# Kernel optimization log

Measured on AMD Instinct MI355X. Metric: run time of the kernel, lower is better.

The kernel has to match this reference:

```python
import jax, jax.numpy as jnp
import numpy as np

B, S, D, H = 8, 512, 2048, 16
DOWN, UP, R = 512, 2048, 512
HD = D // H        # 128, used only in the additive scale
VHD = UP // H      # 128, content head dim / value head dim
BASE = 10000.0


def _rope_tables(head_dim):
    # Faithful to source: positions span arange(head_dim), NOT max_len.
    pos = jnp.arange(head_dim, dtype=jnp.float32)
    div = jnp.exp(jnp.arange(0, head_dim, 2, dtype=jnp.float32) * (-np.log(BASE) / head_dim))
    theta = jnp.outer(pos, div)          # [head_dim, head_dim//2]
    return jnp.sin(theta), jnp.cos(theta)


def _apply_rope(q, num_heads, head_dim):
    # q: [B, S, num_heads*head_dim] -> [B, num_heads, S, head_dim] with interleaved rotation
    b, s, _ = q.shape
    q = q.reshape(b, s, num_heads, head_dim).transpose(0, 2, 1, 3)
    sin, cos = _rope_tables(head_dim)
    sin = sin[:s][None, None]            # [1,1,S,head_dim//2]
    cos = cos[:s][None, None]
    q_ = q.reshape(b, num_heads, s, head_dim // 2, 2)
    q1, q2 = q_[..., 0], q_[..., 1]
    o1 = q1 * cos - q2 * sin
    o2 = q2 * cos + q1 * sin
    return jnp.stack([o1, o2], axis=-1).reshape(b, num_heads, s, head_dim)


def setup_inputs() -> dict:
    key = jax.random.key(0)
    ks = jax.random.split(key, 18)
    w = lambda k, shp: jax.random.normal(k, shp, jnp.float32) * 0.02
    return {
        "X":    jax.random.normal(ks[0], (B, S, D), jnp.float32),
        "Wdq":  w(ks[1], (D, DOWN)),      "bdq":  w(ks[2], (DOWN,)),
        "Wdkv": w(ks[3], (D, DOWN)),      "bdkv": w(ks[4], (DOWN,)),
        "Wuq":  w(ks[5], (DOWN, UP)),     "buq":  w(ks[6], (UP,)),
        "Wuk":  w(ks[7], (DOWN, UP)),     "buk":  w(ks[8], (UP,)),
        "Wuv":  w(ks[9], (DOWN, UP)),     "buv":  w(ks[10], (UP,)),
        "Wqr":  w(ks[11], (DOWN, R * H)), "bqr":  w(ks[12], (R * H,)),
        "Wkr":  w(ks[13], (D, R)),        "bkr":  w(ks[14], (R,)),
        "Wfc":  w(ks[15], (VHD * H, D)),  "bfc":  w(ks[16], (D,)),
    }


def reference(X, Wdq, bdq, Wdkv, bdkv, Wuq, buq, Wuk, buk, Wuv, buv,
              Wqr, bqr, Wkr, bkr, Wfc, bfc):
    b, s, _ = X.shape
    c_q = X @ Wdq + bdq                                  # [B,S,DOWN]
    c_kv = X @ Wdkv + bdkv                               # [B,S,DOWN]
    q_c = (c_q @ Wuq + buq).reshape(b, s, H, VHD).transpose(0, 2, 1, 3)   # [B,H,S,VHD]
    k_c = (c_kv @ Wuk + buk).reshape(b, s, H, VHD).transpose(0, 2, 1, 3)
    v_c = (c_kv @ Wuv + buv).reshape(b, s, H, VHD).transpose(0, 2, 1, 3)
    q_r = _apply_rope(c_q @ Wqr + bqr, H, R)             # [B,H,S,R]
    k_r = _apply_rope(X @ Wkr + bkr, 1, R)               # [B,1,S,R]
    q = jnp.concatenate([q_c, q_r], axis=-1)             # [B,H,S,VHD+R]
    k = jnp.concatenate([k_c, jnp.broadcast_to(k_r, (b, H, s, R))], axis=-1)
    scale = HD ** 0.5 + R ** 0.5                         # additive scale, as in source
    scores = jnp.einsum('bhqd,bhkd->bhqk', q, k) / scale
    attn = jax.nn.softmax(scores, axis=-1)               # dropout: eval mode (identity)
    o = jnp.einsum('bhqk,bhkd->bhqd', attn, v_c).transpose(0, 2, 1, 3).reshape(b, s, H * VHD)
    return o @ Wfc + bfc
```

## Files before the change

### kernel.cpp

```cpp
#include <hip/hip_runtime.h>
#include <hip/hip_bf16.h>
#include <stdint.h>

typedef unsigned short u16;
typedef short bf16x8 __attribute__((ext_vector_type(8)));
typedef float f32x4 __attribute__((ext_vector_type(4)));

__device__ __forceinline__ float us2f(u16 u) {
    union { unsigned int i; float f; } x;
    x.i = ((unsigned int)u) << 16;
    return x.f;
}

__device__ __forceinline__ u16 f2us(float f) {
    union { float f; unsigned int i; } x; x.f = f;
    unsigned int lsb = (x.i >> 16) & 1u;
    x.i += 0x7FFFu + lsb;
    return (u16)(x.i >> 16);
}

__device__ __forceinline__ void gl_lds16(const u16* g, u16* l) {
    __builtin_amdgcn_global_load_lds(
        (const __attribute__((address_space(1))) void*)(uintptr_t)(const void*)g,
        (__attribute__((address_space(3))) void*)(uintptr_t)(void*)l,
        16, 0, 0);
}

#define FLAG_ROPE2  1
#define FLAG_TRANS2 4
#define FLAG_F32OUT 8

struct GArgs {
    const u16 *A0, *B0, *B0r2;
    int K0;
    const float* bias;
    void* C; void* C2;
    int colSplit;
};

template <int LDA0, int LDB0, int LDC, int LDC2, int FLAGS>
__global__ __launch_bounds__(256)
void gemm_mfma(GArgs g)
{
    __shared__ u16 As[128 * 64];
    __shared__ u16 Bs[128 * 64];

    const int t    = threadIdx.x;
    const int lane = t & 63;
    const int w    = t >> 6;
    const int wm   = w >> 1, wn = w & 1;
    const int m0   = blockIdx.y * 128;
    const int n0   = blockIdx.x * 128;
    const bool r2  = (n0 >= g.colSplit);

    const int srow = t >> 3;
    const int sp   = t & 7;
    u16* dA = As + t * 8;
    u16* dB = Bs + t * 8;

    const int lr = lane & 15;
    const int jj = lane >> 4;

    f32x4 acc[4][4];
#pragma unroll
    for (int i = 0; i < 4; ++i)
#pragma unroll
        for (int j = 0; j < 4; ++j)
            acc[i][j] = (f32x4){0.f, 0.f, 0.f, 0.f};

    {
        const u16* A = g.A0;
        const u16* B = r2 ? g.B0r2 - (long)g.colSplit * LDB0 : g.B0;
        const u16* gA[4];
        const u16* gB[4];
#pragma unroll
        for (int r = 0; r < 4; ++r) {
            int row = r * 32 + srow;
            int gc  = (sp - row) & 7;
            gA[r] = A + (long)(m0 + row) * LDA0 + gc * 8;
            gB[r] = B + (long)(n0 + row) * LDB0 + gc * 8;
        }
        for (int kt = 0; kt < g.K0; kt += 64) {
#pragma unroll
            for (int r = 0; r < 4; ++r) {
                gl_lds16(gA[r], dA + r * 2048);
                gl_lds16(gB[r], dB + r * 2048);
                gA[r] += 64; gB[r] += 64;
            }
            __syncthreads();
#pragma unroll
            for (int s = 0; s < 2; ++s) {
                bf16x8 af[4], bfr[4];
#pragma unroll
                for (int mi = 0; mi < 4; ++mi) {
                    int row  = wm * 64 + mi * 16 + lr;
                    int slot = (s * 4 + jj + row) & 7;
                    af[mi] = *(const bf16x8*)&As[row * 64 + slot * 8];
                }
#pragma unroll
                for (int ni = 0; ni < 4; ++ni) {
                    int row  = wn * 64 + ni * 16 + lr;
                    int slot = (s * 4 + jj + row) & 7;
                    bfr[ni] = *(const bf16x8*)&Bs[row * 64 + slot * 8];
                }
#pragma unroll
                for (int mi = 0; mi < 4; ++mi)
#pragma unroll
                    for (int ni = 0; ni < 4; ++ni)
                        acc[mi][ni] = __builtin_amdgcn_mfma_f32_16x16x32_bf16(
                            af[mi], bfr[ni], acc[mi][ni], 0, 0, 0);
            }
            __syncthreads();
        }
    }

    const int eCol0 = n0 + wn * 64 + lr;
    const int eRow0 = m0 + wm * 64 + jj * 4;
    const bool oddc = lane & 1;

    if (g.bias) {
#pragma unroll
        for (int ni = 0; ni < 4; ++ni) {
            float bv = g.bias[eCol0 + ni * 16];
#pragma unroll
            for (int mi = 0; mi < 4; ++mi) {
                acc[mi][ni][0] += bv; acc[mi][ni][1] += bv;
                acc[mi][ni][2] += bv; acc[mi][ni][3] += bv;
            }
        }
    }

    if (!r2) {
#pragma unroll
        for (int mi = 0; mi < 4; ++mi)
#pragma unroll
            for (int ni = 0; ni < 4; ++ni) {
                int rowb = eRow0 + mi * 16;
                int colg = eCol0 + ni * 16;
                if (FLAGS & FLAG_F32OUT) {
                    float* cp = (float*)g.C;
#pragma unroll
                    for (int i = 0; i < 4; ++i)
                        cp[(long)(rowb + i) * LDC + colg] = acc[mi][ni][i];
                } else {
                    u16* cp = (u16*)g.C;
#pragma unroll
                    for (int i = 0; i < 4; ++i)
                        cp[(long)(rowb + i) * LDC + colg] = f2us(acc[mi][ni][i]);
                }
            }
    } else if (FLAGS & FLAG_ROPE2) {
        const float base_s = (float)(eRow0 & 511);
#pragma unroll
        for (int ni = 0; ni < 4; ++ni) {
            int col2 = eCol0 + ni * 16 - g.colSplit;
            int rp   = (col2 & 511) & ~1;
            float f  = __expf(-9.2103403719761836f * (float)rp * (1.0f / 512.0f));
            float s1, c1, s16, c16, sb, cb;
            __sincosf(f, &s1, &c1);
            __sincosf(16.0f * f, &s16, &c16);
            __sincosf(base_s * f, &sb, &cb);
            float cm = cb, sm = sb;
#pragma unroll
            for (int mi = 0; mi < 4; ++mi) {
                f32x4 v = acc[mi][ni];
                float cr = cm, sr = sm;
#pragma unroll
                for (int i = 0; i < 4; ++i) {
                    float other = __shfl_xor(v[i], 1, 64);
                    v[i] = oddc ? (v[i] * cr + other * sr)
                                : (v[i] * cr - other * sr);
                    float cn = cr * c1 - sr * s1;
                    sr = sr * c1 + cr * s1; cr = cn;
                }
                int rowb = eRow0 + mi * 16;
                u16* cp = (u16*)g.C2;
#pragma unroll
                for (int i = 0; i < 4; ++i)
                    cp[(long)(rowb + i) * LDC2 + col2] = f2us(v[i]);
                float cn = cm * c16 - sm * s16;
                sm = sm * c16 + cm * s16; cm = cn;
            }
        }
    } else {
#pragma unroll
        for (int mi = 0; mi < 4; ++mi)
#pragma unroll
            for (int ni = 0; ni < 4; ++ni) {
                int rowb = eRow0 + mi * 16;
                int col2 = eCol0 + ni * 16 - g.colSplit;
                if (FLAGS & FLAG_TRANS2) {
                    u16* cp = (u16*)g.C2 + (long)col2 * LDC2 + rowb;
                    ushort4 o4;
                    o4.x = f2us(acc[mi][ni][0]); o4.y = f2us(acc[mi][ni][1]);
                    o4.z = f2us(acc[mi][ni][2]); o4.w = f2us(acc[mi][ni][3]);
                    *(ushort4*)cp = o4;
                } else {
                    u16* cp = (u16*)g.C2;
#pragma unroll
                    for (int i = 0; i < 4; ++i)
                        cp[(long)(rowb + i) * LDC2 + col2] = f2us(acc[mi][ni][i]);
                }
            }
    }
}

__global__ __launch_bounds__(256, 2)
void attn_fused(const u16* __restrict__ qc, const u16* __restrict__ kc,
                const u16* __restrict__ qr, const u16* __restrict__ kr,
                const u16* __restrict__ vt, u16* __restrict__ o)
{
    __shared__ u16 As[128 * 64];
    __shared__ u16 Bs[128 * 64];
    __shared__ u16 Ps[128 * 136];
    __shared__ float l_sum[128];

    const int t    = threadIdx.x;
    const int lane = t & 63;
    const int w    = t >> 6;
    const int wm   = w >> 1, wn = w & 1;
    const int m0   = blockIdx.x * 128;
    const int z    = blockIdx.y;
    const int bb   = z >> 4, h = z & 15;

    if (t < 128) l_sum[t] = 0.f;

    const int srow = t >> 3;
    const int sp   = t & 7;
    u16* dA = As + t * 8;
    u16* dB = Bs + t * 8;
    int rrow[4], rgc[4];
#pragma unroll
    for (int r = 0; r < 4; ++r) {
        rrow[r] = r * 32 + srow;
        rgc[r]  = (sp - rrow[r]) & 7;
    }

    const int lr = lane & 15;
    const int jj = lane >> 4;

    const u16* gqc[4];
    const u16* gqr[4];
#pragma unroll
    for (int r = 0; r < 4; ++r) {
        gqc[r] = qc + (long)(bb * 512 + m0 + rrow[r]) * 2048 + h * 128 + rgc[r] * 8;
        gqr[r] = qr + (long)(bb * 512 + m0 + rrow[r]) * 8192 + h * 512 + rgc[r] * 8;
    }

    f32x4 acc_o[4][4];
#pragma unroll
    for (int i = 0; i < 4; ++i)
#pragma unroll
        for (int j = 0; j < 4; ++j) acc_o[i][j] = (f32x4){0.f, 0.f, 0.f, 0.f};

    const float scale = 1.0f / 33.941125496954285f;

    for (int nt = 0; nt < 4; ++nt) {
        const int n0k = nt * 128;

        f32x4 acc_s[4][4];
#pragma unroll
        for (int i = 0; i < 4; ++i)
#pragma unroll
            for (int j = 0; j < 4; ++j) acc_s[i][j] = (f32x4){0.f, 0.f, 0.f, 0.f};

        const u16* pa[4];
        const u16* pb[4];
#pragma unroll
        for (int r = 0; r < 4; ++r) {
            pa[r] = gqc[r];
            pb[r] = kc + (long)(bb * 512 + n0k + rrow[r]) * 2048 + h * 128 + rgc[r] * 8;
        }
        for (int seg = 0; seg < 2; ++seg) {
            int iters = seg == 0 ? 2 : 8;
            for (int kt = 0; kt < iters; ++kt) {
#pragma unroll
                for (int r = 0; r < 4; ++r) {
                    gl_lds16(pa[r], dA + r * 2048);
                    gl_lds16(pb[r], dB + r * 2048);
                    pa[r] += 64; pb[r] += 64;
                }
                __syncthreads();
#pragma unroll
                for (int s = 0; s < 2; ++s) {
                    bf16x8 af[4], bfr[4];
#pragma unroll
                    for (int mi = 0; mi < 4; ++mi) {
                        int row  = wm * 64 + mi * 16 + lr;
                        int slot = (s * 4 + jj + row) & 7;
                        af[mi] = *(const bf16x8*)&As[row * 64 + slot * 8];
                    }
#pragma unroll
                    for (int ni = 0; ni < 4; ++ni) {
                        int row  = wn * 64 + ni * 16 + lr;
                        int slot = (s * 4 + jj + row) & 7;
                        bfr[ni] = *(const bf16x8*)&Bs[row * 64 + slot * 8];
                    }
#pragma unroll
                    for (int mi = 0; mi < 4; ++mi)
#pragma unroll
                        for (int ni = 0; ni < 4; ++ni)
                            acc_s[mi][ni] = __builtin_amdgcn_mfma_f32_16x16x32_bf16(
                                af[mi], bfr[ni], acc_s[mi][ni], 0, 0, 0);
                }
                __syncthreads();
            }
            if (seg == 0) {
#pragma unroll
                for (int r = 0; r < 4; ++r) {
                    pa[r] = gqr[r];
                    pb[r] = kr + (long)(bb * 512 + n0k + rrow[r]) * 1536 + rgc[r] * 8;
                }
            }
        }

#pragma unroll
        for (int mi = 0; mi < 4; ++mi) {
            float rowpart[4] = {0.f, 0.f, 0.f, 0.f};
#pragma unroll
            for (int ni = 0; ni < 4; ++ni) {
                f32x4 v = acc_s[mi][ni];
                int colP = wn * 64 + ni * 16 + lr;
#pragma unroll
                for (int i = 0; i < 4; ++i) {
                    float e = __expf(v[i] * scale);
                    rowpart[i] += e;
                    int rowP = wm * 64 + mi * 16 + jj * 4 + i;
                    Ps[rowP * 136 + colP] = f2us(e);
                }
            }
#pragma unroll
            for (int i = 0; i < 4; ++i) {
                float s4 = rowpart[i];
                s4 += __shfl_xor(s4, 1, 64);
                s4 += __shfl_xor(s4, 2, 64);
                s4 += __shfl_xor(s4, 4, 64);
                s4 += __shfl_xor(s4, 8, 64);
                if ((lane & 15) == 0)
                    atomicAdd(&l_sum[wm * 64 + mi * 16 + jj * 4 + i], s4);
            }
        }

        const u16* pv[4];
#pragma unroll
        for (int r = 0; r < 4; ++r)
            pv[r] = vt + (long)(h * 128 + rrow[r]) * 4096 + bb * 512 + n0k + rgc[r] * 8;
        for (int kt = 0; kt < 2; ++kt) {
#pragma unroll
            for (int r = 0; r < 4; ++r) {
                gl_lds16(pv[r], dB + r * 2048);
                pv[r] += 64;
            }
            __syncthreads();
#pragma unroll
            for (int s = 0; s < 2; ++s) {
                bf16x8 af[4], bfr[4];
#pragma unroll
                for (int mi = 0; mi < 4; ++mi) {
                    int row = wm * 64 + mi * 16 + lr;
                    af[mi] = *(const bf16x8*)&Ps[row * 136 + kt * 64 + s * 32 + jj * 8];
                }
#pragma unroll
                for (int ni = 0; ni < 4; ++ni) {
                    int row  = wn * 64 + ni * 16 + lr;
                    int slot = (s * 4 + jj + row) & 7;
                    bfr[ni] = *(const bf16x8*)&Bs[row * 64 + slot * 8];
                }
#pragma unroll
                for (int mi = 0; mi < 4; ++mi)
#pragma unroll
                    for (int ni = 0; ni < 4; ++ni)
                        acc_o[mi][ni] = __builtin_amdgcn_mfma_f32_16x16x32_bf16(
                            af[mi], bfr[ni], acc_o[mi][ni], 0, 0, 0);
            }
            __syncthreads();
        }
    }

#pragma unroll
    for (int mi = 0; mi < 4; ++mi) {
#pragma unroll
        for (int i = 0; i < 4; ++i) {
            int row = wm * 64 + mi * 16 + jj * 4 + i;
            float linv = 1.0f / l_sum[row];
            long grow = (long)(bb * 512 + m0 + row) * 2048 + h * 128;
#pragma unroll
            for (int ni = 0; ni < 4; ++ni) {
                int colc = wn * 64 + ni * 16 + lr;
                o[grow + colc] = f2us(acc_o[mi][ni][i] * linv);
            }
        }
    }
}

__global__ __launch_bounds__(256)
void conv_f32_bf16(const float* __restrict__ in, u16* __restrict__ out)
{
    int i = blockIdx.x * 256 + threadIdx.x;
    float4 v = ((const float4*)in)[i];
    ushort4 o;
    o.x = f2us(v.x); o.y = f2us(v.y); o.z = f2us(v.z); o.w = f2us(v.w);
    ((ushort4*)out)[i] = o;
}

struct TC3 { const float* in0; const float* in1; const float* in2;
             u16* out; long outStride; int K; int N; };

__global__ __launch_bounds__(256)
void tconv3(TC3 a)
{
    __shared__ float tile[32][33];
    const float* in = blockIdx.z == 0 ? a.in0 : (blockIdx.z == 1 ? a.in1 : a.in2);
    u16* out = a.out + blockIdx.z * a.outStride;
    int n0 = blockIdx.x * 32, k0 = blockIdx.y * 32;
    int c = threadIdx.x & 31, r0 = threadIdx.x >> 5;
#pragma unroll
    for (int j = 0; j < 4; ++j) {
        int r = r0 + j * 8;
        tile[r][c] = in[(long)(k0 + r) * a.N + n0 + c];
    }
    __syncthreads();
#pragma unroll
    for (int j = 0; j < 4; ++j) {
        int r = r0 + j * 8;
        out[(long)(n0 + r) * a.K + k0 + c] = f2us(tile[c][r]);
    }
}

extern "C" void kernel_launch(void* const* d_in, const int* in_sizes, int n_in,
                              void* d_out, int out_size, void* d_ws, size_t ws_size,
                              hipStream_t stream)
{
    (void)in_sizes; (void)n_in; (void)out_size; (void)ws_size;

    const float* X    = (const float*)d_in[0];
    const float* Wdq  = (const float*)d_in[1];  const float* bdq  = (const float*)d_in[2];
    const float* Wdkv = (const float*)d_in[3];  const float* bdkv = (const float*)d_in[4];
    const float* Wuq  = (const float*)d_in[5];  const float* buq  = (const float*)d_in[6];
    const float* Wuk  = (const float*)d_in[7];  const float* buk  = (const float*)d_in[8];
    const float* Wuv  = (const float*)d_in[9];  const float* buv  = (const float*)d_in[10];
    const float* Wqr  = (const float*)d_in[11]; const float* bqr  = (const float*)d_in[12];
    const float* Wkr  = (const float*)d_in[13]; const float* bkr  = (const float*)d_in[14];
    const float* Wfc  = (const float*)d_in[15]; const float* bfc  = (const float*)d_in[16];
    float* out = (float*)d_out;

    u16* ws = (u16*)d_ws;
    u16* Xb     = ws;
    u16* Wc1    = Xb   + 8388608;
    u16* Wc2    = Wc1  + 3145728;
    u16* Wqr_t  = Wc2  + 3145728;
    u16* Wfc_t  = Wqr_t + 4194304;
    u16* ckk    = Wfc_t + 4194304;
    u16* q_c    = ckk  + 6291456;
    u16* k_c    = q_c  + 8388608;
    u16* v_t    = k_c  + 8388608;
    u16* q_r    = v_t  + 8388608;
    u16* o      = q_r  + 33554432;
    float* biasD = (float*)(o + 8388608);
    float* biasQ = biasD + 1536;
    float* biasK = biasQ + 10240;

    dim3 blk(256, 1, 1);

    conv_f32_bf16<<<8192, blk, 0, stream>>>(X, Xb);
    {   TC3 a{Wdq, Wdkv, Wkr, Wc1, 1048576, 2048, 512};
        tconv3<<<dim3(16, 64, 3), blk, 0, stream>>>(a); }
    {   TC3 a{Wuq, Wuk, Wuv, Wc2, 1048576, 512, 2048};
        tconv3<<<dim3(64, 16, 3), blk, 0, stream>>>(a); }
    {   TC3 a{Wqr, nullptr, nullptr, Wqr_t, 0, 512, 8192};
        tconv3<<<dim3(256, 16, 1), blk, 0, stream>>>(a); }
    {   TC3 a{Wfc, nullptr, nullptr, Wfc_t, 0, 2048, 2048};
        tconv3<<<dim3(64, 64, 1), blk, 0, stream>>>(a); }
    hipMemcpyAsync(biasD,        bdq,  512 * 4,  hipMemcpyDeviceToDevice, stream);
    hipMemcpyAsync(biasD + 512,  bdkv, 512 * 4,  hipMemcpyDeviceToDevice, stream);
    hipMemcpyAsync(biasD + 1024, bkr,  512 * 4,  hipMemcpyDeviceToDevice, stream);
    hipMemcpyAsync(biasQ,        buq,  2048 * 4, hipMemcpyDeviceToDevice, stream);
    hipMemcpyAsync(biasQ + 2048, bqr,  8192 * 4, hipMemcpyDeviceToDevice, stream);
    hipMemcpyAsync(biasK,        buk,  2048 * 4, hipMemcpyDeviceToDevice, stream);
    hipMemcpyAsync(biasK + 2048, buv,  2048 * 4, hipMemcpyDeviceToDevice, stream);

    const int NOSPLIT = 1 << 30;

    {
        GArgs a{};
        a.A0 = Xb; a.B0 = Wc1; a.B0r2 = Wc1 + 2l * 1048576; a.K0 = 2048;
        a.bias = biasD; a.C = ckk; a.C2 = ckk + 1024;
        a.colSplit = 1024;
        gemm_mfma<2048, 2048, 1536, 1536, FLAG_ROPE2>
            <<<dim3(12, 32, 1), blk, 0, stream>>>(a);
    }
    {
        GArgs a{};
        a.A0 = ckk; a.B0 = Wc2; a.B0r2 = Wqr_t; a.K0 = 512;
        a.bias = biasQ; a.C = q_c; a.C2 = q_r;
        a.colSplit = 2048;
        gemm_mfma<1536, 512, 2048, 8192, FLAG_ROPE2>
            <<<dim3(80, 32, 1), blk, 0, stream>>>(a);
    }
    {
        GArgs a{};
        a.A0 = ckk + 512; a.B0 = Wc2 + 1048576; a.B0r2 = Wc2 + 2l * 1048576;
        a.K0 = 512;
        a.bias = biasK; a.C = k_c; a.C2 = v_t;
        a.colSplit = 2048;
        gemm_mfma<1536, 512, 2048, 4096, FLAG_TRANS2>
            <<<dim3(32, 32, 1), blk, 0, stream>>>(a);
    }

    attn_fused<<<dim3(4, 128, 1), blk, 0, stream>>>(
        q_c, k_c, q_r, ckk + 1024, v_t, o);

    {
        GArgs a{};
        a.A0 = o; a.B0 = Wfc_t; a.B0r2 = Wfc_t; a.K0 = 2048;
        a.bias = bfc; a.C = out; a.C2 = out;
        a.colSplit = NOSPLIT;
        gemm_mfma<2048, 2048, 2048, 1, FLAG_F32OUT>
            <<<dim3(16, 32, 1), blk, 0, stream>>>(a);
    }
}
```

Before: 466.7 us.

## Merge weight transposes and bias copies into single launches; XCD-aware attention block mapping

Four transpose-convert launches are merged into one flat-grid kernel, and seven device-to-device bias memcpys are replaced by a single gather kernel. Both cut launch and memcpy overhead. The attention kernel also remaps its block index so that all query tiles and heads of one batch land on the same XCD, which should improve L2 reuse of K/V. The remap assumes the attention grid is 4x128 and round-robin dispatch across eight XCDs.

```diff
diff --git a/kernel.cpp b/kernel.cpp
--- a/kernel.cpp
+++ b/kernel.cpp
@@ -219,8 +219,12 @@
     const int lane = t & 63;
     const int w    = t >> 6;
     const int wm   = w >> 1, wn = w & 1;
-    const int m0   = blockIdx.x * 128;
-    const int z    = blockIdx.y;
+
+    const int flat = blockIdx.x + (blockIdx.y << 2);
+    const int xcd  = flat & 7;
+    const int j    = flat >> 3;
+    const int m0   = (j >> 4) * 128;
+    const int z    = xcd * 16 + (j & 15);
     const int bb   = z >> 4, h = z & 15;
 
     if (t < 128) l_sum[t] = 0.f;
@@ -251,7 +255,7 @@
 #pragma unroll
     for (int i = 0; i < 4; ++i)
 #pragma unroll
-        for (int j = 0; j < 4; ++j) acc_o[i][j] = (f32x4){0.f, 0.f, 0.f, 0.f};
+        for (int j2 = 0; j2 < 4; ++j2) acc_o[i][j2] = (f32x4){0.f, 0.f, 0.f, 0.f};
 
     const float scale = 1.0f / 33.941125496954285f;
 
@@ -262,7 +266,7 @@
 #pragma unroll
         for (int i = 0; i < 4; ++i)
 #pragma unroll
-            for (int j = 0; j < 4; ++j) acc_s[i][j] = (f32x4){0.f, 0.f, 0.f, 0.f};
+            for (int j2 = 0; j2 < 4; ++j2) acc_s[i][j2] = (f32x4){0.f, 0.f, 0.f, 0.f};
 
         const u16* pa[4];
         const u16* pb[4];
@@ -403,27 +407,69 @@
     ((ushort4*)out)[i] = o;
 }
 
-struct TC3 { const float* in0; const float* in1; const float* in2;
-             u16* out; long outStride; int K; int N; };
+struct TCAll {
+    const float *Wdq, *Wdkv, *Wkr, *Wuq, *Wuk, *Wuv, *Wqr, *Wfc;
+    u16 *Wc1, *Wc2, *Wqr_t, *Wfc_t;
+};
 
 __global__ __launch_bounds__(256)
-void tconv3(TC3 a)
+void tconv_all(TCAll a)
 {
     __shared__ float tile[32][33];
-    const float* in = blockIdx.z == 0 ? a.in0 : (blockIdx.z == 1 ? a.in1 : a.in2);
-    u16* out = a.out + blockIdx.z * a.outStride;
-    int n0 = blockIdx.x * 32, k0 = blockIdx.y * 32;
-    int c = threadIdx.x & 31, r0 = threadIdx.x >> 5;
+    const int bid = blockIdx.x;
+    const float* in; u16* out; int K, N, nx, ny;
+    if (bid < 3072) {
+        int z = bid >> 10, rem = bid & 1023;
+        in = z == 0 ? a.Wdq : (z == 1 ? a.Wdkv : a.Wkr);
+        out = a.Wc1 + z * 1048576;
+        K = 2048; N = 512; nx = rem & 15; ny = rem >> 4;
+    } else if (bid < 6144) {
+        int l = bid - 3072, z = l >> 10, rem = l & 1023;
+        in = z == 0 ? a.Wuq : (z == 1 ? a.Wuk : a.Wuv);
+        out = a.Wc2 + z * 1048576;
+        K = 512; N = 2048; nx = rem & 63; ny = rem >> 6;
+    } else if (bid < 10240) {
+        int l = bid - 6144;
+        in = a.Wqr; out = a.Wqr_t;
+        K = 512; N = 8192; nx = l & 255; ny = l >> 8;
+    } else {
+        int l = bid - 10240;
+        in = a.Wfc; out = a.Wfc_t;
+        K = 2048; N = 2048; nx = l & 63; ny = l >> 6;
+    }
+    const int n0 = nx * 32, k0 = ny * 32;
+    const int c = threadIdx.x & 31, r0 = threadIdx.x >> 5;
 #pragma unroll
     for (int j = 0; j < 4; ++j) {
         int r = r0 + j * 8;
-        tile[r][c] = in[(long)(k0 + r) * a.N + n0 + c];
+        tile[r][c] = in[(long)(k0 + r) * N + n0 + c];
     }
     __syncthreads();
 #pragma unroll
     for (int j = 0; j < 4; ++j) {
         int r = r0 + j * 8;
-        out[(long)(n0 + r) * a.K + k0 + c] = f2us(tile[c][r]);
+        out[(long)(n0 + r) * K + k0 + c] = f2us(tile[c][r]);
+    }
+}
+
+struct BG {
+    const float *bdq, *bdkv, *bkr, *buq, *bqr, *buk, *buv;
+    float *biasD, *biasQ, *biasK;
+};
+
+__global__ __launch_bounds__(256)
+void bias_gather(BG a)
+{
+    int i = blockIdx.x * 256 + threadIdx.x;
+    if (i < 1536) {
+        float v = i < 512 ? a.bdq[i] : (i < 1024 ? a.bdkv[i - 512] : a.bkr[i - 1024]);
+        a.biasD[i] = v;
+    } else if (i < 11776) {
+        int j = i - 1536;
+        a.biasQ[j] = j < 2048 ? a.buq[j] : a.bqr[j - 2048];
+    } else {
+        int j = i - 11776;
+        a.biasK[j] = j < 2048 ? a.buk[j] : a.buv[j - 2048];
     }
 }
 
@@ -463,21 +509,11 @@
     dim3 blk(256, 1, 1);
 
     conv_f32_bf16<<<8192, blk, 0, stream>>>(X, Xb);
-    {   TC3 a{Wdq, Wdkv, Wkr, Wc1, 1048576, 2048, 512};
-        tconv3<<<dim3(16, 64, 3), blk, 0, stream>>>(a); }
-    {   TC3 a{Wuq, Wuk, Wuv, Wc2, 1048576, 512, 2048};
-        tconv3<<<dim3(64, 16, 3), blk, 0, stream>>>(a); }
-    {   TC3 a{Wqr, nullptr, nullptr, Wqr_t, 0, 512, 8192};
-        tconv3<<<dim3(256, 16, 1), blk, 0, stream>>>(a); }
-    {   TC3 a{Wfc, nullptr, nullptr, Wfc_t, 0, 2048, 2048};
-        tconv3<<<dim3(64, 64, 1), blk, 0, stream>>>(a); }
-    hipMemcpyAsync(biasD,        bdq,  512 * 4,  hipMemcpyDeviceToDevice, stream);
-    hipMemcpyAsync(biasD + 512,  bdkv, 512 * 4,  hipMemcpyDeviceToDevice, stream);
-    hipMemcpyAsync(biasD + 1024, bkr,  512 * 4,  hipMemcpyDeviceToDevice, stream);
-    hipMemcpyAsync(biasQ,        buq,  2048 * 4, hipMemcpyDeviceToDevice, stream);
-    hipMemcpyAsync(biasQ + 2048, bqr,  8192 * 4, hipMemcpyDeviceToDevice, stream);
-    hipMemcpyAsync(biasK,        buk,  2048 * 4, hipMemcpyDeviceToDevice, stream);
-    hipMemcpyAsync(biasK + 2048, buv,  2048 * 4, hipMemcpyDeviceToDevice, stream);
+    {   TCAll a{Wdq, Wdkv, Wkr, Wuq, Wuk, Wuv, Wqr, Wfc,
+                Wc1, Wc2, Wqr_t, Wfc_t};
+        tconv_all<<<14336, blk, 0, stream>>>(a); }
+    {   BG a{bdq, bdkv, bkr, buq, bqr, buk, buv, biasD, biasQ, biasK};
+        bias_gather<<<62, blk, 0, stream>>>(a); }
 
     const int NOSPLIT = 1 << 30;
 
```

After: 433.0 us. 7.2% less time.
